# Kernel optimization log

Hardware: AMD Instinct MI355X
Metric: run time of the kernel (lower is better)

Reference implementation:

```python
import jax, jax.numpy as jnp
import numpy as np

N, E, D, L, B, T = 50000, 600000, 128, 7, 512, 10
ATOM_DIMS = [119, 4, 12, 12, 10, 6, 6, 2, 2]
BOND_DIMS = [5, 6, 2]
MSG_EPS = 1e-7   # GENConv message epsilon
BN_EPS = 1e-5    # torch BatchNorm1d eps


def _offsets(dims):
    return jnp.asarray(np.concatenate([[0], np.cumsum(dims[:-1])]), dtype=jnp.int32)


def setup_inputs():
    key = jax.random.key(0)
    k = lambda i: jax.random.fold_in(key, i)
    x = jnp.stack([jax.random.randint(k(i), (N,), 0, d) for i, d in enumerate(ATOM_DIMS)], axis=1)
    edge_attr = jnp.stack([jax.random.randint(k(100 + i), (E,), 0, d) for i, d in enumerate(BOND_DIMS)], axis=1)
    edge_index = jax.random.randint(k(200), (2, E), 0, N)
    batch = jnp.sort(jax.random.randint(k(201), (N,), 0, B))
    atom_table = 0.1 * jax.random.normal(k(300), (sum(ATOM_DIMS), D), jnp.float32)
    bond_table = 0.1 * jax.random.normal(k(301), (sum(BOND_DIMS), D), jnp.float32)
    norm_gamma = jnp.ones((L, D), jnp.float32)
    norm_beta = jnp.zeros((L, D), jnp.float32)
    t = 0.1 * jnp.ones((L,), jnp.float32)
    mlp_w1 = 0.05 * jax.random.normal(k(302), (L, D, 2 * D), jnp.float32)
    mlp_b1 = jnp.zeros((L, 2 * D), jnp.float32)
    mlp_bng = jnp.ones((L, 2 * D), jnp.float32)
    mlp_bnb = jnp.zeros((L, 2 * D), jnp.float32)
    mlp_w2 = 0.05 * jax.random.normal(k(303), (L, 2 * D, D), jnp.float32)
    mlp_b2 = jnp.zeros((L, D), jnp.float32)
    pred_w = 0.05 * jax.random.normal(k(304), (D, T), jnp.float32)
    pred_b = jnp.zeros((T,), jnp.float32)
    return dict(x=x, edge_index=edge_index, edge_attr=edge_attr, batch=batch,
                atom_offsets=_offsets(ATOM_DIMS), bond_offsets=_offsets(BOND_DIMS),
                atom_table=atom_table, bond_table=bond_table,
                norm_gamma=norm_gamma, norm_beta=norm_beta, t=t,
                mlp_w1=mlp_w1, mlp_b1=mlp_b1, mlp_bng=mlp_bng, mlp_bnb=mlp_bnb,
                mlp_w2=mlp_w2, mlp_b2=mlp_b2, pred_w=pred_w, pred_b=pred_b)


def _batchnorm(z, gamma, beta):
    # training-mode BatchNorm1d: batch stats, biased variance
    mu = z.mean(0)
    var = z.var(0)
    return (z - mu) * jax.lax.rsqrt(var + BN_EPS) * gamma + beta


def _genconv(h, ea, src, dst, t, w1, b1, g1, bt1, w2, b2):
    # GENConv: message = relu(x_j + edge_attr) + eps; softmax aggregation with temperature t
    msg = jax.nn.relu(h[src] + ea) + MSG_EPS                 # [E, D]
    logits = msg * t
    m = jax.ops.segment_max(logits, dst, num_segments=N)     # [N, D]
    m = jax.lax.stop_gradient(jnp.where(jnp.isfinite(m), m, 0.0))
    e = jnp.exp(logits - m[dst])
    denom = jax.ops.segment_sum(e, dst, num_segments=N)
    alpha = e / (denom[dst] + 1e-16)
    aggr = jax.ops.segment_sum(msg * alpha, dst, num_segments=N)  # [N, D]
    out = h + aggr                                           # update: x_r + aggr
    z = _batchnorm(out @ w1 + b1, g1, bt1)                   # MLP: D -> 2D (BN, ReLU) -> D
    return jax.nn.relu(z) @ w2 + b2


def reference(x, edge_index, edge_attr, batch, atom_offsets, bond_offsets,
              atom_table, bond_table, norm_gamma, norm_beta, t,
              mlp_w1, mlp_b1, mlp_bng, mlp_bnb, mlp_w2, mlp_b2, pred_w, pred_b):
    h = atom_table[x + atom_offsets[None, :]].sum(1)               # [N, D] AtomEncoder
    ea = bond_table[edge_attr + bond_offsets[None, :]].sum(1)      # [E, D] BondEncoder
    src, dst = edge_index[0], edge_index[1]
    # first layer: bare conv
    h = _genconv(h, ea, src, dst, t[0], mlp_w1[0], mlp_b1[0], mlp_bng[0], mlp_bnb[0], mlp_w2[0], mlp_b2[0])
    # remaining layers: res+ blocks (norm -> act -> conv -> residual); dropout=0
    for i in range(1, L):
        r = jax.nn.relu(_batchnorm(h, norm_gamma[i], norm_beta[i]))
        r = _genconv(r, ea, src, dst, t[i], mlp_w1[i], mlp_b1[i], mlp_bng[i], mlp_bnb[i], mlp_w2[i], mlp_b2[i])
        h = h + r
    h = _batchnorm(h, norm_gamma[0], norm_beta[0])                 # layers[0].norm
    # global mean pool over graphs
    sums = jax.ops.segment_sum(h, batch, num_segments=B)
    cnts = jax.ops.segment_sum(jnp.ones((N,), h.dtype), batch, num_segments=B)
    graph_emb = sums / jnp.maximum(cnts, 1.0)[:, None]
    return graph_emb @ pred_w + pred_b                             # [B, T]
```

## Files before the change

### kernel.cpp

```cpp
#include <hip/hip_runtime.h>
#include <hip/hip_bf16.h>

#define N_NODES 50000
#define N_EDGES 600000
#define D 128
#define D2 256
#define NGRAPH 512
#define NTARGET 10
#define NSB 49
#define NSLOT 32

static constexpr float MSG_EPS_F = 1e-7f;
static constexpr float BN_EPS_F  = 1e-5f;

typedef _Float16 half8 __attribute__((ext_vector_type(8)));
typedef _Float16 half4v __attribute__((ext_vector_type(4)));
typedef float f32x4 __attribute__((ext_vector_type(4)));
#define MFMA16(a, b, c) __builtin_amdgcn_mfma_f32_16x16x32_f16(a, b, c, 0, 0, 0)

__global__ __launch_bounds__(256) void k_encode(
    const int* __restrict__ x, const int* __restrict__ aoff,
    const float* __restrict__ atab, float* __restrict__ h,
    _Float16* __restrict__ rh, int* __restrict__ deg) {
  int tid = blockIdx.x * 256 + threadIdx.x;
  if (tid < N_NODES) deg[tid] = 0;
  int n = tid >> 5, f4 = (tid & 31) << 2;
  if (n >= N_NODES) return;
  float4 acc = make_float4(0.f, 0.f, 0.f, 0.f);
#pragma unroll
  for (int i = 0; i < 9; ++i) {
    int row = x[n * 9 + i] + aoff[i];
    float4 v = *(const float4*)&atab[row * D + f4];
    acc.x += v.x; acc.y += v.y; acc.z += v.z; acc.w += v.w;
  }
  *(float4*)&h[(size_t)n * D + f4] = acc;
  half4v o = {(_Float16)acc.x, (_Float16)acc.y, (_Float16)acc.z, (_Float16)acc.w};
  *(half4v*)&rh[(size_t)n * D + f4] = o;
}

__global__ __launch_bounds__(128) void k_combo(
    const int* __restrict__ boff, const float* __restrict__ btab,
    _Float16* __restrict__ comboh) {
  int c = blockIdx.x, t = threadIdx.x;
  int a0 = c / 12, a1 = (c % 12) / 2, a2 = c % 2;
  comboh[c * D + t] = (_Float16)(btab[(boff[0] + a0) * D + t] +
                                 btab[(boff[1] + a1) * D + t] +
                                 btab[(boff[2] + a2) * D + t]);
}

__global__ __launch_bounds__(256) void k_packW(
    const float* __restrict__ w1, const float* __restrict__ w2,
    _Float16* __restrict__ w1p, _Float16* __restrict__ w2p) {
  int t = blockIdx.x * 256 + threadIdx.x;
  if (t < 7 * 4096) {
    int lane = t & 63, ntAll = (t >> 6) & 15, kc = (t >> 10) & 3, l = t >> 12;
    int q = lane >> 4, c = ntAll * 16 + (lane & 15);
    int kbase = kc * 32 + q * 8;
    const float* W = w1 + (size_t)l * D * D2;
    half8 v;
#pragma unroll
    for (int j = 0; j < 8; ++j) v[j] = (_Float16)W[(size_t)(kbase + j) * D2 + c];
    *(half8*)&w1p[(size_t)t * 8] = v;
  } else {
    int u = t - 7 * 4096;
    if (u < 7 * 4096) {
      int lane = u & 63, nt = (u >> 6) & 7, kcAll = (u >> 9) & 7, l = u >> 12;
      int q = lane >> 4, c = nt * 16 + (lane & 15);
      int kbase = kcAll * 32 + q * 8;
      const float* W = w2 + (size_t)l * D2 * D;
      half8 v;
#pragma unroll
      for (int j = 0; j < 8; ++j) v[j] = (_Float16)W[(size_t)(kbase + j) * D + c];
      *(half8*)&w2p[(size_t)u * 8] = v;
    }
  }
}

__global__ __launch_bounds__(256) void k_degree(
    const int* __restrict__ ei, int* __restrict__ deg) {
  int e = blockIdx.x * 256 + threadIdx.x;
  if (e >= N_EDGES) return;
  atomicAdd(&deg[ei[N_EDGES + e]], 1);
}

__global__ __launch_bounds__(1024) void k_scan1(
    const int* __restrict__ deg, int* __restrict__ excl, int* __restrict__ bsum) {
  __shared__ int tmp[1024];
  int t = threadIdx.x, i = blockIdx.x * 1024 + t;
  int v = (i < N_NODES) ? deg[i] : 0;
  tmp[t] = v;
  __syncthreads();
  for (int off = 1; off < 1024; off <<= 1) {
    int add = (t >= off) ? tmp[t - off] : 0;
    __syncthreads();
    tmp[t] += add;
    __syncthreads();
  }
  if (i < N_NODES) excl[i] = tmp[t] - v;
  if (t == 1023) bsum[blockIdx.x] = tmp[1023];
}

__global__ __launch_bounds__(64) void k_scan2(int* __restrict__ bsum) {
  __shared__ int s[64];
  int t = threadIdx.x;
  int v = (t < NSB) ? bsum[t] : 0;
  s[t] = v;
  __syncthreads();
  for (int off = 1; off < 64; off <<= 1) {
    int add = (t >= off) ? s[t - off] : 0;
    __syncthreads();
    s[t] += add;
    __syncthreads();
  }
  if (t < NSB) bsum[t] = s[t] - v;
}

__global__ __launch_bounds__(256) void k_scan3(
    const int* __restrict__ excl, const int* __restrict__ bsum,
    int* __restrict__ rowptr, int* __restrict__ cursor) {
  int i = blockIdx.x * 256 + threadIdx.x;
  if (i < N_NODES) {
    int v = excl[i] + bsum[i >> 10];
    rowptr[i] = v;
    cursor[i] = v;
  }
  if (i == N_NODES) rowptr[N_NODES] = N_EDGES;
}

__global__ __launch_bounds__(256) void k_scatter(
    const int* __restrict__ ei, const int* __restrict__ eattr,
    int* __restrict__ cursor, int* __restrict__ payload) {
  int e = blockIdx.x * 256 + threadIdx.x;
  if (e >= N_EDGES) return;
  int src = ei[e], dst = ei[N_EDGES + e];
  int cid = eattr[e * 3 + 0] * 12 + eattr[e * 3 + 1] * 2 + eattr[e * 3 + 2];
  int pos = atomicAdd(&cursor[dst], 1);
  payload[pos] = (src << 6) | cid;
}

__global__ __launch_bounds__(256) void k_gbounds(
    const int* __restrict__ batch, int* __restrict__ gstart) {
  int n = blockIdx.x * 256 + threadIdx.x;
  if (n >= N_NODES) return;
  int b0 = batch[n];
  int b1 = (n + 1 < N_NODES) ? batch[n + 1] : NGRAPH;
  for (int bb = b0 + 1; bb <= b1; ++bb) gstart[bb] = n + 1;
  if (n == 0)
    for (int bb = 0; bb <= b0; ++bb) gstart[bb] = 0;
}

__global__ __launch_bounds__(256) void k_prenorm(
    const float* __restrict__ h, const float* __restrict__ statHs,
    const float* __restrict__ gamma, const float* __restrict__ beta,
    _Float16* __restrict__ rh) {
  __shared__ float sH[256];
  int t = threadIdx.x;
  {
    float a = 0.f;
#pragma unroll
    for (int s = 0; s < NSLOT; ++s) a += statHs[s * 256 + t];
    sH[t] = a;
  }
  __syncthreads();
  int tid = blockIdx.x * 256 + t;
  int n = tid >> 5, f4 = (t & 31) << 2;
  if (n >= N_NODES) return;
  const float invN = 1.0f / (float)N_NODES;
  float4 s  = *(const float4*)&sH[f4];
  float4 sq = *(const float4*)&sH[D + f4];
  float4 g  = *(const float4*)&gamma[f4];
  float4 b  = *(const float4*)&beta[f4];
  float4 hv = *(const float4*)&h[(size_t)n * D + f4];
  float mu = s.x * invN, var = sq.x * invN - mu * mu;
  float ox = fmaxf((hv.x - mu) * rsqrtf(var + BN_EPS_F) * g.x + b.x, 0.f);
  mu = s.y * invN; var = sq.y * invN - mu * mu;
  float oy = fmaxf((hv.y - mu) * rsqrtf(var + BN_EPS_F) * g.y + b.y, 0.f);
  mu = s.z * invN; var = sq.z * invN - mu * mu;
  float oz = fmaxf((hv.z - mu) * rsqrtf(var + BN_EPS_F) * g.z + b.z, 0.f);
  mu = s.w * invN; var = sq.w * invN - mu * mu;
  float ow = fmaxf((hv.w - mu) * rsqrtf(var + BN_EPS_F) * g.w + b.w, 0.f);
  half4v o = {(_Float16)ox, (_Float16)oy, (_Float16)oz, (_Float16)ow};
  *(half4v*)&rh[(size_t)n * D + f4] = o;
}

__global__ __launch_bounds__(256) void k_aggr(
    const _Float16* __restrict__ rh, const int* __restrict__ rowptr,
    const int* __restrict__ payload, const _Float16* __restrict__ comboh,
    const float* __restrict__ tptr, int l, _Float16* __restrict__ xh,
    float* __restrict__ stat1s, float* __restrict__ statHs) {
  if (blockIdx.x < NSLOT) {
    float* z1 = stat1s + blockIdx.x * 512;
    float* zH = statHs + blockIdx.x * 256;
    for (int j = threadIdx.x; j < 768; j += 256) {
      if (j < 512) z1[j] = 0.f;
      else zH[j - 512] = 0.f;
    }
  }
  int tid = blockIdx.x * 256 + threadIdx.x;
  int dst = tid >> 4, f8 = (tid & 15) << 3;
  if (dst >= N_NODES) return;
  float tv = tptr[l];
  int s = rowptr[dst], e = rowptr[dst + 1];
  float den[8], S[8];
#pragma unroll
  for (int j = 0; j < 8; ++j) { den[j] = 0.f; S[j] = 0.f; }
  int i = s;
  for (; i + 1 < e; i += 2) {
    int p0 = payload[i], p1 = payload[i + 1];
    half8 r0 = *(const half8*)&rh[(size_t)(p0 >> 6) * D + f8];
    half8 r1 = *(const half8*)&rh[(size_t)(p1 >> 6) * D + f8];
    half8 c0 = *(const half8*)&comboh[(p0 & 63) * D + f8];
    half8 c1 = *(const half8*)&comboh[(p1 & 63) * D + f8];
#pragma unroll
    for (int j = 0; j < 8; ++j) {
      float m0 = fmaxf((float)r0[j] + (float)c0[j], 0.f) + MSG_EPS_F;
      float m1 = fmaxf((float)r1[j] + (float)c1[j], 0.f) + MSG_EPS_F;
      float e0 = __expf(m0 * tv), e1 = __expf(m1 * tv);
      den[j] += e0 + e1;
      S[j] += m0 * e0 + m1 * e1;
    }
  }
  if (i < e) {
    int p0 = payload[i];
    half8 r0 = *(const half8*)&rh[(size_t)(p0 >> 6) * D + f8];
    half8 c0 = *(const half8*)&comboh[(p0 & 63) * D + f8];
#pragma unroll
    for (int j = 0; j < 8; ++j) {
      float m0 = fmaxf((float)r0[j] + (float)c0[j], 0.f) + MSG_EPS_F;
      float e0 = __expf(m0 * tv);
      den[j] += e0;
      S[j] += m0 * e0;
    }
  }
  half8 ro = *(const half8*)&rh[(size_t)dst * D + f8];
  half8 o;
#pragma unroll
  for (int j = 0; j < 8; ++j)
    o[j] = (_Float16)((float)ro[j] + S[j] / (den[j] + 1e-16f));
  *(half8*)&xh[(size_t)dst * D + f8] = o;
}

__global__ __launch_bounds__(256) void k_gemm1(
    const _Float16* __restrict__ xh, const _Float16* __restrict__ w1p,
    const float* __restrict__ b1, _Float16* __restrict__ z1h,
    float* __restrict__ stat1s) {
  __shared__ __align__(16) _Float16 Af[512 * 8];
  int tid = threadIdx.x;
  int row0 = blockIdx.x * 32;
  int slot = blockIdx.x & (NSLOT - 1);

#pragma unroll
  for (int s0 = 0; s0 < 2; ++s0) {
    int s = s0 * 256 + tid;
    int kc = s >> 7, mt = (s >> 6) & 1, l2 = s & 63;
    int row = row0 + mt * 16 + (l2 & 15);
    int kb = kc * 32 + ((l2 >> 4) << 3);
    half8 v;
    if (row < N_NODES) {
      v = *(const half8*)&xh[(size_t)row * D + kb];
    } else {
#pragma unroll
      for (int j = 0; j < 8; ++j) v[j] = (_Float16)0.f;
    }
    *(half8*)&Af[s * 8] = v;
  }
  __syncthreads();

  int wv = tid >> 6, ln = tid & 63;
  f32x4 acc[2][4];
#pragma unroll
  for (int i = 0; i < 2; ++i)
#pragma unroll
    for (int j = 0; j < 4; ++j) acc[i][j] = (f32x4){0.f, 0.f, 0.f, 0.f};

#pragma unroll
  for (int kc = 0; kc < 4; ++kc) {
    half8 a0 = *(half8*)&Af[((kc * 2 + 0) * 64 + ln) * 8];
    half8 a1 = *(half8*)&Af[((kc * 2 + 1) * 64 + ln) * 8];
#pragma unroll
    for (int nt = 0; nt < 4; ++nt) {
      int ntAll = wv * 4 + nt;
      half8 b = *(const half8*)&w1p[((size_t)(kc * 16 + ntAll) * 64 + ln) * 8];
      acc[0][nt] = MFMA16(a0, b, acc[0][nt]);
      acc[1][nt] = MFMA16(a1, b, acc[1][nt]);
    }
  }
  int lq = ln >> 4, lc = ln & 15;
  float cs[4], cq[4];
#pragma unroll
  for (int nt = 0; nt < 4; ++nt) { cs[nt] = 0.f; cq[nt] = 0.f; }
#pragma unroll
  for (int nt = 0; nt < 4; ++nt) {
    int col = (wv * 4 + nt) * 16 + lc;
    float bias = b1[col];
#pragma unroll
    for (int mt = 0; mt < 2; ++mt) {
      int rbase = row0 + mt * 16 + lq * 4;
#pragma unroll
      for (int rg = 0; rg < 4; ++rg) {
        int row = rbase + rg;
        if (row < N_NODES) {
          float z = acc[mt][nt][rg] + bias;
          z1h[(size_t)row * D2 + col] = (_Float16)z;
          cs[nt] += z; cq[nt] += z * z;
        }
      }
    }
  }
#pragma unroll
  for (int nt = 0; nt < 4; ++nt) {
    float v = cs[nt], q = cq[nt];
    v += __shfl_xor(v, 16); v += __shfl_xor(v, 32);
    q += __shfl_xor(q, 16); q += __shfl_xor(q, 32);
    if (lq == 0) {
      int col = (wv * 4 + nt) * 16 + lc;
      atomicAdd(&stat1s[slot * 512 + col], v);
      atomicAdd(&stat1s[slot * 512 + 256 + col], q);
    }
  }
}

__global__ __launch_bounds__(256) void k_gemm2(
    const _Float16* __restrict__ z1h, const float* __restrict__ stat1s,
    const float* __restrict__ g1, const float* __restrict__ bt1,
    const _Float16* __restrict__ w2p, const float* __restrict__ b2,
    float* __restrict__ h, int residual, float* __restrict__ statHs) {
  __shared__ __align__(16) _Float16 Af[1024 * 8];
  __shared__ float s1[512];
  const float invN = 1.0f / (float)N_NODES;
  int tid = threadIdx.x;
  int row0 = blockIdx.x * 32;
  int slot = blockIdx.x & (NSLOT - 1);

#pragma unroll
  for (int jj = 0; jj < 2; ++jj) {
    int j = jj * 256 + tid;
    float a = 0.f;
#pragma unroll
    for (int s = 0; s < NSLOT; ++s) a += stat1s[s * 512 + j];
    s1[j] = a;
  }
  __syncthreads();

#pragma unroll
  for (int s0 = 0; s0 < 4; ++s0) {
    int s = s0 * 256 + tid;
    int kcAll = s >> 7, mt = (s >> 6) & 1, l2 = s & 63;
    int row = row0 + mt * 16 + (l2 & 15);
    int kb = kcAll * 32 + ((l2 >> 4) << 3);
    half8 v;
    if (row < N_NODES) {
      half8 z = *(const half8*)&z1h[(size_t)row * D2 + kb];
#pragma unroll
      for (int j = 0; j < 8; ++j) {
        float mu = s1[kb + j] * invN;
        float isg = rsqrtf(s1[256 + kb + j] * invN - mu * mu + BN_EPS_F) * g1[kb + j];
        v[j] = (_Float16)fmaxf(((float)z[j] - mu) * isg + bt1[kb + j], 0.f);
      }
    } else {
#pragma unroll
      for (int j = 0; j < 8; ++j) v[j] = (_Float16)0.f;
    }
    *(half8*)&Af[s * 8] = v;
  }
  __syncthreads();

  int wv = tid >> 6, ln = tid & 63;
  f32x4 acc[2][2];
#pragma unroll
  for (int i = 0; i < 2; ++i)
#pragma unroll
    for (int j = 0; j < 2; ++j) acc[i][j] = (f32x4){0.f, 0.f, 0.f, 0.f};

#pragma unroll
  for (int kcAll = 0; kcAll < 8; ++kcAll) {
    half8 a0 = *(half8*)&Af[((kcAll * 2 + 0) * 64 + ln) * 8];
    half8 a1 = *(half8*)&Af[((kcAll * 2 + 1) * 64 + ln) * 8];
#pragma unroll
    for (int nt = 0; nt < 2; ++nt) {
      half8 b = *(const half8*)&w2p[((size_t)(kcAll * 8 + wv * 2 + nt) * 64 + ln) * 8];
      acc[0][nt] = MFMA16(a0, b, acc[0][nt]);
      acc[1][nt] = MFMA16(a1, b, acc[1][nt]);
    }
  }
  int lq = ln >> 4, lc = ln & 15;
  float cs[2], cq[2];
#pragma unroll
  for (int nt = 0; nt < 2; ++nt) { cs[nt] = 0.f; cq[nt] = 0.f; }
#pragma unroll
  for (int nt = 0; nt < 2; ++nt) {
    int col = (wv * 2 + nt) * 16 + lc;
    float bias = b2[col];
#pragma unroll
    for (int mt = 0; mt < 2; ++mt) {
      int rbase = row0 + mt * 16 + lq * 4;
#pragma unroll
      for (int rg = 0; rg < 4; ++rg) {
        int row = rbase + rg;
        if (row < N_NODES) {
          float v = acc[mt][nt][rg] + bias;
          if (residual) v += h[(size_t)row * D + col];
          h[(size_t)row * D + col] = v;
          cs[nt] += v; cq[nt] += v * v;
        }
      }
    }
  }
#pragma unroll
  for (int nt = 0; nt < 2; ++nt) {
    float v = cs[nt], q = cq[nt];
    v += __shfl_xor(v, 16); v += __shfl_xor(v, 32);
    q += __shfl_xor(q, 16); q += __shfl_xor(q, 32);
    if (lq == 0) {
      int col = (wv * 2 + nt) * 16 + lc;
      atomicAdd(&statHs[slot * 256 + col], v);
      atomicAdd(&statHs[slot * 256 + 128 + col], q);
    }
  }
}

__global__ __launch_bounds__(256) void k_poolpred(
    const float* __restrict__ h, const int* __restrict__ gstart,
    const float* __restrict__ statHs, const float* __restrict__ gamma,
    const float* __restrict__ beta, const float* __restrict__ pw,
    const float* __restrict__ pb, float* __restrict__ out) {
  __shared__ float sH[256];
  __shared__ float emb[128];
  __shared__ float4 red[256];
  int b = blockIdx.x, tid = threadIdx.x;
  {
    float a = 0.f;
#pragma unroll
    for (int s = 0; s < NSLOT; ++s) a += statHs[s * 256 + tid];
    sH[tid] = a;
  }
  int fl = (tid & 31) << 2, ns = tid >> 5;
  int gs = gstart[b], ge = gstart[b + 1];
  float4 acc = make_float4(0.f, 0.f, 0.f, 0.f);
  for (int n = gs + ns; n < ge; n += 8) {
    float4 v = *(const float4*)&h[(size_t)n * D + fl];
    acc.x += v.x; acc.y += v.y; acc.z += v.z; acc.w += v.w;
  }
  red[tid] = acc;
  __syncthreads();
  if (ns < 4) {
    float4 o = red[tid + 128];
    acc.x += o.x; acc.y += o.y; acc.z += o.z; acc.w += o.w;
    red[tid] = acc;
  }
  __syncthreads();
  if (ns < 2) {
    float4 o = red[tid + 64];
    acc.x += o.x; acc.y += o.y; acc.z += o.z; acc.w += o.w;
    red[tid] = acc;
  }
  __syncthreads();
  if (ns == 0) {
    float4 o = red[tid + 32];
    acc.x += o.x; acc.y += o.y; acc.z += o.z; acc.w += o.w;
    const float invN = 1.0f / (float)N_NODES;
    float inv = (ge > gs) ? 1.0f / (float)(ge - gs) : 0.f;
    float av[4] = {acc.x, acc.y, acc.z, acc.w};
#pragma unroll
    for (int j = 0; j < 4; ++j) {
      int k = fl + j;
      float mu = sH[k] * invN;
      float var = sH[D + k] * invN - mu * mu;
      emb[k] = (ge > gs)
          ? (av[j] * inv - mu) * rsqrtf(var + BN_EPS_F) * gamma[k] + beta[k]
          : 0.f;
    }
  }
  __syncthreads();
  if (tid < NTARGET) {
    float o = pb[tid];
    for (int k = 0; k < D; ++k) o += emb[k] * pw[k * NTARGET + tid];
    out[b * NTARGET + tid] = o;
  }
}

extern "C" void kernel_launch(void* const* d_in, const int* in_sizes, int n_in,
                              void* d_out, int out_size, void* d_ws, size_t ws_size,
                              hipStream_t stream) {
  const int* x      = (const int*)d_in[0];
  const int* ei     = (const int*)d_in[1];
  const int* eattr  = (const int*)d_in[2];
  const int* batch  = (const int*)d_in[3];
  const int* aoff   = (const int*)d_in[4];
  const int* boff   = (const int*)d_in[5];
  const float* atab = (const float*)d_in[6];
  const float* btab = (const float*)d_in[7];
  const float* ngam = (const float*)d_in[8];
  const float* nbet = (const float*)d_in[9];
  const float* tptr = (const float*)d_in[10];
  const float* w1   = (const float*)d_in[11];
  const float* b1   = (const float*)d_in[12];
  const float* bng  = (const float*)d_in[13];
  const float* bnb  = (const float*)d_in[14];
  const float* w2   = (const float*)d_in[15];
  const float* b2   = (const float*)d_in[16];
  const float* pw   = (const float*)d_in[17];
  const float* pb   = (const float*)d_in[18];
  float* out = (float*)d_out;

  float* ws = (float*)d_ws;
  const size_t ND = (size_t)N_NODES * D;
  float* h      = ws;
  _Float16* rh  = (_Float16*)(ws + 1 * ND);
  _Float16* xh  = (_Float16*)(ws + 1 * ND + ND / 2);
  _Float16* z1h = (_Float16*)(ws + 2 * ND);
  float* stat1s = ws + 3 * ND;
  float* statHs = stat1s + NSLOT * 512;
  float* psum   = statHs + NSLOT * 256;
  float* comboF = psum + (size_t)NGRAPH * D;
  _Float16* comboh = (_Float16*)comboF;
  _Float16* w1p = (_Float16*)(comboF + 60 * D);
  _Float16* w2p = w1p + 7 * 32768;
  int* ibuf     = (int*)(w2p + 7 * 32768);
  int* rowptr   = ibuf;
  int* cursor   = rowptr + N_NODES + 1;
  int* deg      = cursor + N_NODES;
  int* payload  = deg + N_NODES;
  int* gstart   = payload + N_EDGES;
  int* excl     = gstart + NGRAPH + 1;
  int* bsum     = excl + N_NODES;

  const int nodeBlocks = (N_NODES * 32 + 255) / 256;
  const int aggrBlocks = (N_NODES * 16 + 255) / 256;
  const int edgeThreadBlocks = (N_EDGES + 255) / 256;
  const int nBlocks256 = (N_NODES + 255) / 256;
  const int gRows32 = (N_NODES + 31) / 32;

  k_encode<<<nodeBlocks, 256, 0, stream>>>(x, aoff, atab, h, rh, deg);
  k_combo<<<60, 128, 0, stream>>>(boff, btab, comboh);
  k_packW<<<(2 * 7 * 4096 + 255) / 256, 256, 0, stream>>>(w1, w2, w1p, w2p);
  k_gbounds<<<nBlocks256, 256, 0, stream>>>(batch, gstart);
  k_degree<<<edgeThreadBlocks, 256, 0, stream>>>(ei, deg);
  k_scan1<<<NSB, 1024, 0, stream>>>(deg, excl, bsum);
  k_scan2<<<1, 64, 0, stream>>>(bsum);
  k_scan3<<<(N_NODES + 256) / 256, 256, 0, stream>>>(excl, bsum, rowptr, cursor);
  k_scatter<<<edgeThreadBlocks, 256, 0, stream>>>(ei, eattr, cursor, payload);

  for (int l = 0; l < 7; ++l) {
    if (l > 0)
      k_prenorm<<<nodeBlocks, 256, 0, stream>>>(h, statHs, ngam + l * D, nbet + l * D, rh);
    k_aggr<<<aggrBlocks, 256, 0, stream>>>(rh, rowptr, payload, comboh, tptr, l, xh,
                                           stat1s, statHs);
    k_gemm1<<<gRows32, 256, 0, stream>>>(xh, w1p + (size_t)l * 32768,
                                         b1 + l * D2, z1h, stat1s);
    k_gemm2<<<gRows32, 256, 0, stream>>>(z1h, stat1s, bng + l * D2, bnb + l * D2,
                                         w2p + (size_t)l * 32768, b2 + l * D,
                                         h, l > 0 ? 1 : 0, statHs);
  }

  k_poolpred<<<NGRAPH, 256, 0, stream>>>(h, gstart, statHs, ngam, nbet, pw, pb, out);
}
```

Measured before the change: 909.7 us.

## Fuse prenorm and softmax aggregation into GEMM1, store fp16 copy of h

Merges the per-layer prenorm, aggregation and first GEMM kernels into one k_layer1 kernel. It applies BatchNorm+ReLU on the fly to each gathered neighbor row and writes the aggregated result straight into the GEMM's shared-memory tile. GEMM2 now also writes an fp16 copy of h. Stats buffers become per-layer and are zeroed once with a memset, so zeroing inside kernels is no longer needed. This removes two launches and the rh/xh round trips per layer, but each gathered neighbor now pays extra FMA and max ops, and the aggregation runs on only 32 rows per block.

```diff
diff --git a/kernel.cpp b/kernel.cpp
--- a/kernel.cpp
+++ b/kernel.cpp
@@ -21,7 +21,7 @@
 __global__ __launch_bounds__(256) void k_encode(
     const int* __restrict__ x, const int* __restrict__ aoff,
     const float* __restrict__ atab, float* __restrict__ h,
-    _Float16* __restrict__ rh, int* __restrict__ deg) {
+    _Float16* __restrict__ hh, int* __restrict__ deg) {
   int tid = blockIdx.x * 256 + threadIdx.x;
   if (tid < N_NODES) deg[tid] = 0;
   int n = tid >> 5, f4 = (tid & 31) << 2;
@@ -35,7 +35,7 @@
   }
   *(float4*)&h[(size_t)n * D + f4] = acc;
   half4v o = {(_Float16)acc.x, (_Float16)acc.y, (_Float16)acc.z, (_Float16)acc.w};
-  *(half4v*)&rh[(size_t)n * D + f4] = o;
+  *(half4v*)&hh[(size_t)n * D + f4] = o;
 }
 
 __global__ __launch_bounds__(128) void k_combo(
@@ -149,120 +149,100 @@
     for (int bb = 0; bb <= b0; ++bb) gstart[bb] = 0;
 }
 
-__global__ __launch_bounds__(256) void k_prenorm(
-    const float* __restrict__ h, const float* __restrict__ statHs,
+__global__ __launch_bounds__(256) void k_layer1(
+    const _Float16* __restrict__ hh, const int* __restrict__ rowptr,
+    const int* __restrict__ payload, const _Float16* __restrict__ comboh,
+    const float* __restrict__ tptr, int l,
+    const float* __restrict__ statHsPrev,
     const float* __restrict__ gamma, const float* __restrict__ beta,
-    _Float16* __restrict__ rh) {
-  __shared__ float sH[256];
-  int t = threadIdx.x;
-  {
-    float a = 0.f;
-#pragma unroll
-    for (int s = 0; s < NSLOT; ++s) a += statHs[s * 256 + t];
-    sH[t] = a;
-  }
-  __syncthreads();
-  int tid = blockIdx.x * 256 + t;
-  int n = tid >> 5, f4 = (t & 31) << 2;
-  if (n >= N_NODES) return;
-  const float invN = 1.0f / (float)N_NODES;
-  float4 s  = *(const float4*)&sH[f4];
-  float4 sq = *(const float4*)&sH[D + f4];
-  float4 g  = *(const float4*)&gamma[f4];
-  float4 b  = *(const float4*)&beta[f4];
-  float4 hv = *(const float4*)&h[(size_t)n * D + f4];
-  float mu = s.x * invN, var = sq.x * invN - mu * mu;
-  float ox = fmaxf((hv.x - mu) * rsqrtf(var + BN_EPS_F) * g.x + b.x, 0.f);
-  mu = s.y * invN; var = sq.y * invN - mu * mu;
-  float oy = fmaxf((hv.y - mu) * rsqrtf(var + BN_EPS_F) * g.y + b.y, 0.f);
-  mu = s.z * invN; var = sq.z * invN - mu * mu;
-  float oz = fmaxf((hv.z - mu) * rsqrtf(var + BN_EPS_F) * g.z + b.z, 0.f);
-  mu = s.w * invN; var = sq.w * invN - mu * mu;
-  float ow = fmaxf((hv.w - mu) * rsqrtf(var + BN_EPS_F) * g.w + b.w, 0.f);
-  half4v o = {(_Float16)ox, (_Float16)oy, (_Float16)oz, (_Float16)ow};
-  *(half4v*)&rh[(size_t)n * D + f4] = o;
-}
-
-__global__ __launch_bounds__(256) void k_aggr(
-    const _Float16* __restrict__ rh, const int* __restrict__ rowptr,
-    const int* __restrict__ payload, const _Float16* __restrict__ comboh,
-    const float* __restrict__ tptr, int l, _Float16* __restrict__ xh,
-    float* __restrict__ stat1s, float* __restrict__ statHs) {
-  if (blockIdx.x < NSLOT) {
-    float* z1 = stat1s + blockIdx.x * 512;
-    float* zH = statHs + blockIdx.x * 256;
-    for (int j = threadIdx.x; j < 768; j += 256) {
-      if (j < 512) z1[j] = 0.f;
-      else zH[j - 512] = 0.f;
-    }
-  }
-  int tid = blockIdx.x * 256 + threadIdx.x;
-  int dst = tid >> 4, f8 = (tid & 15) << 3;
-  if (dst >= N_NODES) return;
-  float tv = tptr[l];
-  int s = rowptr[dst], e = rowptr[dst + 1];
-  float den[8], S[8];
-#pragma unroll
-  for (int j = 0; j < 8; ++j) { den[j] = 0.f; S[j] = 0.f; }
-  int i = s;
-  for (; i + 1 < e; i += 2) {
-    int p0 = payload[i], p1 = payload[i + 1];
-    half8 r0 = *(const half8*)&rh[(size_t)(p0 >> 6) * D + f8];
-    half8 r1 = *(const half8*)&rh[(size_t)(p1 >> 6) * D + f8];
-    half8 c0 = *(const half8*)&comboh[(p0 & 63) * D + f8];
-    half8 c1 = *(const half8*)&comboh[(p1 & 63) * D + f8];
-#pragma unroll
-    for (int j = 0; j < 8; ++j) {
-      float m0 = fmaxf((float)r0[j] + (float)c0[j], 0.f) + MSG_EPS_F;
-      float m1 = fmaxf((float)r1[j] + (float)c1[j], 0.f) + MSG_EPS_F;
-      float e0 = __expf(m0 * tv), e1 = __expf(m1 * tv);
-      den[j] += e0 + e1;
-      S[j] += m0 * e0 + m1 * e1;
-    }
-  }
-  if (i < e) {
-    int p0 = payload[i];
-    half8 r0 = *(const half8*)&rh[(size_t)(p0 >> 6) * D + f8];
-    half8 c0 = *(const half8*)&comboh[(p0 & 63) * D + f8];
-#pragma unroll
-    for (int j = 0; j < 8; ++j) {
-      float m0 = fmaxf((float)r0[j] + (float)c0[j], 0.f) + MSG_EPS_F;
-      float e0 = __expf(m0 * tv);
-      den[j] += e0;
-      S[j] += m0 * e0;
-    }
-  }
-  half8 ro = *(const half8*)&rh[(size_t)dst * D + f8];
-  half8 o;
-#pragma unroll
-  for (int j = 0; j < 8; ++j)
-    o[j] = (_Float16)((float)ro[j] + S[j] / (den[j] + 1e-16f));
-  *(half8*)&xh[(size_t)dst * D + f8] = o;
-}
-
-__global__ __launch_bounds__(256) void k_gemm1(
-    const _Float16* __restrict__ xh, const _Float16* __restrict__ w1p,
-    const float* __restrict__ b1, _Float16* __restrict__ z1h,
-    float* __restrict__ stat1s) {
+    const _Float16* __restrict__ w1p, const float* __restrict__ b1,
+    _Float16* __restrict__ z1h, float* __restrict__ stat1s) {
   __shared__ __align__(16) _Float16 Af[512 * 8];
+  __shared__ float bnA[128], bnB[128];
   int tid = threadIdx.x;
   int row0 = blockIdx.x * 32;
   int slot = blockIdx.x & (NSLOT - 1);
-
-#pragma unroll
-  for (int s0 = 0; s0 < 2; ++s0) {
-    int s = s0 * 256 + tid;
-    int kc = s >> 7, mt = (s >> 6) & 1, l2 = s & 63;
-    int row = row0 + mt * 16 + (l2 & 15);
-    int kb = kc * 32 + ((l2 >> 4) << 3);
+  float negcap;
+  if (l > 0) {
+    if (tid < 128) {
+      float s = 0.f, sq = 0.f;
+#pragma unroll
+      for (int sl = 0; sl < NSLOT; ++sl) {
+        s += statHsPrev[sl * 256 + tid];
+        sq += statHsPrev[sl * 256 + 128 + tid];
+      }
+      const float invN = 1.0f / (float)N_NODES;
+      float mu = s * invN, var = sq * invN - mu * mu;
+      float isg = rsqrtf(var + BN_EPS_F) * gamma[tid];
+      bnA[tid] = isg;
+      bnB[tid] = beta[tid] - mu * isg;
+    }
+    negcap = 0.f;
+  } else {
+    if (tid < 128) { bnA[tid] = 1.f; bnB[tid] = 0.f; }
+    negcap = -1e30f;
+  }
+  __syncthreads();
+  float tv = tptr[l];
+  int f8 = (tid & 15) << 3;
+
+#pragma unroll
+  for (int pass = 0; pass < 2; ++pass) {
+    int dl = pass * 16 + (tid >> 4);
+    int dst = row0 + dl;
     half8 v;
-    if (row < N_NODES) {
-      v = *(const half8*)&xh[(size_t)row * D + kb];
+    if (dst < N_NODES) {
+      float a[8], bb[8];
+#pragma unroll
+      for (int j = 0; j < 8; ++j) { a[j] = bnA[f8 + j]; bb[j] = bnB[f8 + j]; }
+      int s = rowptr[dst], e = rowptr[dst + 1];
+      float den[8], S[8];
+#pragma unroll
+      for (int j = 0; j < 8; ++j) { den[j] = 0.f; S[j] = 0.f; }
+      int i = s;
+      for (; i + 1 < e; i += 2) {
+        int p0 = payload[i], p1 = payload[i + 1];
+        half8 h0 = *(const half8*)&hh[(size_t)(p0 >> 6) * D + f8];
+        half8 h1v = *(const half8*)&hh[(size_t)(p1 >> 6) * D + f8];
+        half8 c0 = *(const half8*)&comboh[(p0 & 63) * D + f8];
+        half8 c1 = *(const half8*)&comboh[(p1 & 63) * D + f8];
+#pragma unroll
+        for (int j = 0; j < 8; ++j) {
+          float r0 = fmaxf(fmaf((float)h0[j], a[j], bb[j]), negcap);
+          float r1 = fmaxf(fmaf((float)h1v[j], a[j], bb[j]), negcap);
+          float m0 = fmaxf(r0 + (float)c0[j], 0.f) + MSG_EPS_F;
+          float m1 = fmaxf(r1 + (float)c1[j], 0.f) + MSG_EPS_F;
+          float e0 = __expf(m0 * tv), e1 = __expf(m1 * tv);
+          den[j] += e0 + e1;
+          S[j] += m0 * e0 + m1 * e1;
+        }
+      }
+      if (i < e) {
+        int p0 = payload[i];
+        half8 h0 = *(const half8*)&hh[(size_t)(p0 >> 6) * D + f8];
+        half8 c0 = *(const half8*)&comboh[(p0 & 63) * D + f8];
+#pragma unroll
+        for (int j = 0; j < 8; ++j) {
+          float r0 = fmaxf(fmaf((float)h0[j], a[j], bb[j]), negcap);
+          float m0 = fmaxf(r0 + (float)c0[j], 0.f) + MSG_EPS_F;
+          float e0 = __expf(m0 * tv);
+          den[j] += e0;
+          S[j] += m0 * e0;
+        }
+      }
+      half8 hd = *(const half8*)&hh[(size_t)dst * D + f8];
+#pragma unroll
+      for (int j = 0; j < 8; ++j) {
+        float rd = fmaxf(fmaf((float)hd[j], a[j], bb[j]), negcap);
+        v[j] = (_Float16)(rd + S[j] / (den[j] + 1e-16f));
+      }
     } else {
 #pragma unroll
       for (int j = 0; j < 8; ++j) v[j] = (_Float16)0.f;
     }
-    *(half8*)&Af[s * 8] = v;
+    int kc = f8 >> 5, q = (f8 >> 3) & 3, lrow = dl & 15;
+    int fslot = (kc * 2 + pass) * 64 + q * 16 + lrow;
+    *(half8*)&Af[fslot * 8] = v;
   }
   __syncthreads();
 
@@ -324,7 +304,8 @@
     const _Float16* __restrict__ z1h, const float* __restrict__ stat1s,
     const float* __restrict__ g1, const float* __restrict__ bt1,
     const _Float16* __restrict__ w2p, const float* __restrict__ b2,
-    float* __restrict__ h, int residual, float* __restrict__ statHs) {
+    float* __restrict__ h, _Float16* __restrict__ hh, int residual,
+    float* __restrict__ statHs) {
   __shared__ __align__(16) _Float16 Af[1024 * 8];
   __shared__ float s1[512];
   const float invN = 1.0f / (float)N_NODES;
@@ -401,6 +382,7 @@
           float v = acc[mt][nt][rg] + bias;
           if (residual) v += h[(size_t)row * D + col];
           h[(size_t)row * D + col] = v;
+          hh[(size_t)row * D + col] = (_Float16)v;
           cs[nt] += v; cq[nt] += v * v;
         }
       }
@@ -506,13 +488,12 @@
   float* ws = (float*)d_ws;
   const size_t ND = (size_t)N_NODES * D;
   float* h      = ws;
-  _Float16* rh  = (_Float16*)(ws + 1 * ND);
-  _Float16* xh  = (_Float16*)(ws + 1 * ND + ND / 2);
+  _Float16* hh  = (_Float16*)(ws + 1 * ND);
   _Float16* z1h = (_Float16*)(ws + 2 * ND);
-  float* stat1s = ws + 3 * ND;
-  float* statHs = stat1s + NSLOT * 512;
-  float* psum   = statHs + NSLOT * 256;
-  float* comboF = psum + (size_t)NGRAPH * D;
+  float* statAll = ws + 3 * ND;
+  float* stat1sAll = statAll;
+  float* statHsAll = statAll + 7 * NSLOT * 512;
+  float* comboF = statHsAll + 7 * NSLOT * 256;
   _Float16* comboh = (_Float16*)comboF;
   _Float16* w1p = (_Float16*)(comboF + 60 * D);
   _Float16* w2p = w1p + 7 * 32768;
@@ -526,12 +507,12 @@
   int* bsum     = excl + N_NODES;
 
   const int nodeBlocks = (N_NODES * 32 + 255) / 256;
-  const int aggrBlocks = (N_NODES * 16 + 255) / 256;
   const int edgeThreadBlocks = (N_EDGES + 255) / 256;
   const int nBlocks256 = (N_NODES + 255) / 256;
   const int gRows32 = (N_NODES + 31) / 32;
 
-  k_encode<<<nodeBlocks, 256, 0, stream>>>(x, aoff, atab, h, rh, deg);
+  (void)hipMemsetAsync(statAll, 0, (size_t)7 * NSLOT * (512 + 256) * sizeof(float), stream);
+  k_encode<<<nodeBlocks, 256, 0, stream>>>(x, aoff, atab, h, hh, deg);
   k_combo<<<60, 128, 0, stream>>>(boff, btab, comboh);
   k_packW<<<(2 * 7 * 4096 + 255) / 256, 256, 0, stream>>>(w1, w2, w1p, w2p);
   k_gbounds<<<nBlocks256, 256, 0, stream>>>(batch, gstart);
@@ -542,16 +523,19 @@
   k_scatter<<<edgeThreadBlocks, 256, 0, stream>>>(ei, eattr, cursor, payload);
 
   for (int l = 0; l < 7; ++l) {
-    if (l > 0)
-      k_prenorm<<<nodeBlocks, 256, 0, stream>>>(h, statHs, ngam + l * D, nbet + l * D, rh);
-    k_aggr<<<aggrBlocks, 256, 0, stream>>>(rh, rowptr, payload, comboh, tptr, l, xh,
-                                           stat1s, statHs);
-    k_gemm1<<<gRows32, 256, 0, stream>>>(xh, w1p + (size_t)l * 32768,
-                                         b1 + l * D2, z1h, stat1s);
-    k_gemm2<<<gRows32, 256, 0, stream>>>(z1h, stat1s, bng + l * D2, bnb + l * D2,
-                                         w2p + (size_t)l * 32768, b2 + l * D,
-                                         h, l > 0 ? 1 : 0, statHs);
-  }
-
-  k_poolpred<<<NGRAPH, 256, 0, stream>>>(h, gstart, statHs, ngam, nbet, pw, pb, out);
-}
+    k_layer1<<<gRows32, 256, 0, stream>>>(
+        hh, rowptr, payload, comboh, tptr, l,
+        (l > 0) ? statHsAll + (size_t)(l - 1) * NSLOT * 256 : statHsAll,
+        ngam + l * D, nbet + l * D,
+        w1p + (size_t)l * 32768, b1 + l * D2, z1h,
+        stat1sAll + (size_t)l * NSLOT * 512);
+    k_gemm2<<<gRows32, 256, 0, stream>>>(
+        z1h, stat1sAll + (size_t)l * NSLOT * 512, bng + l * D2, bnb + l * D2,
+        w2p + (size_t)l * 32768, b2 + l * D, h, hh, l > 0 ? 1 : 0,
+        statHsAll + (size_t)l * NSLOT * 256);
+  }
+
+  k_poolpred<<<NGRAPH, 256, 0, stream>>>(h, gstart,
+                                         statHsAll + (size_t)6 * NSLOT * 256,
+                                         ngam, nbet, pw, pb, out);
+}
```

Result: slower. 952.4 us (+4.7%).
